# Performance work log

Hardware: AMD Instinct MI355X
Metric: run time of the kernel (lower is better)

Reference implementation:

```python
import jax, jax.numpy as jnp
import numpy as np

N_NODES = 50000
N_EDGES = 1600000
IN_FEATS = 32
HIDDEN = 64
OUT_FEAT = 64


def setup_inputs() -> dict:
    key = jax.random.key(0)
    ks = jax.random.split(key, 8)
    inputs = jax.random.normal(ks[0], (N_NODES, IN_FEATS), dtype=jnp.float32)
    edge_weights = jax.random.uniform(ks[1], (N_EDGES, 1), dtype=jnp.float32)
    src = jax.random.randint(ks[2], (N_EDGES,), 0, N_NODES, dtype=jnp.int32)
    dst = jax.random.randint(ks[3], (N_EDGES,), 0, N_NODES, dtype=jnp.int32)
    W1 = jax.random.normal(ks[4], (IN_FEATS, HIDDEN), dtype=jnp.float32) / np.sqrt(IN_FEATS)
    b1 = jnp.zeros((HIDDEN,), dtype=jnp.float32)
    W2 = jax.random.normal(ks[5], (HIDDEN + IN_FEATS, OUT_FEAT), dtype=jnp.float32) / np.sqrt(HIDDEN + IN_FEATS)
    b2 = jnp.zeros((OUT_FEAT,), dtype=jnp.float32)
    return {"inputs": inputs, "edge_weights": edge_weights, "src": src, "dst": dst,
            "W1": W1, "b1": b1, "W2": W2, "b2": b2}


def _weighted_graph_conv(x, W, b, src, dst, ew, src_norm, dst_norm, n_nodes):
    # x: [N, Din] -> [N, Dout]
    x = x @ W                               # dense projection
    x = x * src_norm                        # D_out^{-1/2} scaling at source
    m = x[src] * ew                         # [E, Dout] gather * edge weight
    h = jax.ops.segment_sum(m, dst, num_segments=n_nodes)  # scatter-sum at dest
    return h * dst_norm + b                 # D_in^{-1/2} scaling + bias


def reference(inputs, edge_weights, src, dst, W1, b1, W2, b2):
    n = inputs.shape[0]
    ones = jnp.ones((src.shape[0],), dtype=jnp.float32)
    out_deg = jax.ops.segment_sum(ones, src, num_segments=n)
    in_deg = jax.ops.segment_sum(ones, dst, num_segments=n)
    src_norm = jnp.clip(out_deg, 1.0, None)[:, None] ** -0.5  # [N,1]
    dst_norm = jnp.clip(in_deg, 1.0, None)[:, None] ** -0.5   # [N,1]

    h = _weighted_graph_conv(inputs, W1, b1, src, dst, edge_weights, src_norm, dst_norm, n)
    h = jax.nn.relu(h)
    reminder = jnp.concatenate([h, inputs], axis=-1)  # re-inject input features
    h = _weighted_graph_conv(reminder, W2, b2, src, dst, edge_weights, src_norm, dst_norm, n)
    h = jax.nn.relu(h)
    # torch F.normalize(p=2, dim=-1, eps=1e-12)
    norm = jnp.linalg.norm(h, axis=-1, keepdims=True)
    return h / jnp.maximum(norm, 1e-12)
```

## Files before the change

### kernel.cpp

```cpp
#include <hip/hip_runtime.h>
#include <math.h>


#define BUK 128
#define BUK_SHIFT 7
#define FSH 256
#define SS 128
#define HIST_BS 512
#define NBUK_MAX 512
#define MAX_LDS_BYTES 131072
#define PNB 16

#define SCAN_BS 256
#define SCAN_ITEMS 4
#define SCAN_CHUNK (SCAN_BS * SCAN_ITEMS)

__device__ __forceinline__ unsigned short f2bf(float f) {
    unsigned u = __float_as_uint(f);
    return (unsigned short)((u + 0x7fffu + ((u >> 16) & 1u)) >> 16);
}
__device__ __forceinline__ float bf2f(unsigned short h) {
    return __uint_as_float((unsigned)h << 16);
}

__device__ __forceinline__ float edge_gather(const int* __restrict__ offsets,
                                             const unsigned* __restrict__ edata,
                                             const unsigned short* __restrict__ xp,
                                             int n, int lane) {
    int beg = offsets[n];
    int end = offsets[n + 1];
    float a0 = 0.f, a1 = 0.f, a2 = 0.f, a3 = 0.f;
    for (int p = beg; p < end; p += 64) {
        int cnt = min(64, end - p);
        unsigned eb = (p + lane < end) ? edata[p + lane] : 0u;
        int k = 0;
        for (; k + 7 < cnt; k += 8) {
            unsigned e0 = __builtin_amdgcn_readlane(eb, k);
            unsigned e1 = __builtin_amdgcn_readlane(eb, k + 1);
            unsigned e2 = __builtin_amdgcn_readlane(eb, k + 2);
            unsigned e3 = __builtin_amdgcn_readlane(eb, k + 3);
            unsigned e4 = __builtin_amdgcn_readlane(eb, k + 4);
            unsigned e5 = __builtin_amdgcn_readlane(eb, k + 5);
            unsigned e6 = __builtin_amdgcn_readlane(eb, k + 6);
            unsigned e7 = __builtin_amdgcn_readlane(eb, k + 7);
            float v0 = bf2f(xp[(size_t)(e0 & 0xffffu) * 64 + lane]);
            float v1 = bf2f(xp[(size_t)(e1 & 0xffffu) * 64 + lane]);
            float v2 = bf2f(xp[(size_t)(e2 & 0xffffu) * 64 + lane]);
            float v3 = bf2f(xp[(size_t)(e3 & 0xffffu) * 64 + lane]);
            float v4 = bf2f(xp[(size_t)(e4 & 0xffffu) * 64 + lane]);
            float v5 = bf2f(xp[(size_t)(e5 & 0xffffu) * 64 + lane]);
            float v6 = bf2f(xp[(size_t)(e6 & 0xffffu) * 64 + lane]);
            float v7 = bf2f(xp[(size_t)(e7 & 0xffffu) * 64 + lane]);
            a0 = fmaf(v0, bf2f((unsigned short)(e0 >> 16)), a0);
            a1 = fmaf(v1, bf2f((unsigned short)(e1 >> 16)), a1);
            a2 = fmaf(v2, bf2f((unsigned short)(e2 >> 16)), a2);
            a3 = fmaf(v3, bf2f((unsigned short)(e3 >> 16)), a3);
            a0 = fmaf(v4, bf2f((unsigned short)(e4 >> 16)), a0);
            a1 = fmaf(v5, bf2f((unsigned short)(e5 >> 16)), a1);
            a2 = fmaf(v6, bf2f((unsigned short)(e6 >> 16)), a2);
            a3 = fmaf(v7, bf2f((unsigned short)(e7 >> 16)), a3);
        }
        for (; k < cnt; ++k) {
            unsigned e0 = __builtin_amdgcn_readlane(eb, k);
            a0 = fmaf(bf2f(xp[(size_t)(e0 & 0xffffu) * 64 + lane]),
                      bf2f((unsigned short)(e0 >> 16)), a0);
        }
    }
    return (a0 + a1) + (a2 + a3);
}

__global__ void hist_src_kernel(const int* __restrict__ src, unsigned* __restrict__ partial_s,
                                int E, int NW4, int sliceS) {
    extern __shared__ unsigned h[];
    for (int i = threadIdx.x; i < NW4; i += blockDim.x) h[i] = 0u;
    __syncthreads();
    int s = blockIdx.x;
    int beg = s * sliceS, end = min(beg + sliceS, E);
    for (int e = beg + (int)threadIdx.x; e < end; e += blockDim.x) {
        int v = src[e];
        atomicAdd(&h[v >> 2], 1u << (8 * (v & 3)));
    }
    __syncthreads();
    unsigned* o = partial_s + (size_t)s * NW4;
    for (int i = threadIdx.x; i < NW4; i += blockDim.x) o[i] = h[i];
}

__global__ void reduce_src_kernel(const unsigned* __restrict__ partial_s,
                                  float* __restrict__ srcn, int N, int NW4) {
    int w = blockIdx.x * blockDim.x + threadIdx.x;
    if (w >= NW4) return;
    unsigned run = 0;
#pragma unroll 4
    for (int s = 0; s < SS; ++s) run += partial_s[(size_t)s * NW4 + w];
    int n0 = 4 * w;
#pragma unroll
    for (int k = 0; k < 4; ++k) {
        int n = n0 + k;
        if (n < N) srcn[n] = rsqrtf(fmaxf((float)((run >> (8 * k)) & 0xffu), 1.0f));
    }
}

__global__ void count_kernel(const int* __restrict__ dst, int* __restrict__ cntmat,
                             int E, int L, int NBUK) {
    __shared__ int c[NBUK_MAX];
    for (int i = threadIdx.x; i < NBUK; i += blockDim.x) c[i] = 0;
    __syncthreads();
    int s = blockIdx.x;
    int beg = s * L, end = min(beg + L, E);
    for (int e = beg + (int)threadIdx.x; e < end; e += blockDim.x)
        atomicAdd(&c[dst[e] >> BUK_SHIFT], 1);
    __syncthreads();
    for (int b = threadIdx.x; b < NBUK; b += blockDim.x)
        cntmat[(size_t)b * FSH + s] = c[b];
}

__global__ void scan_partial(const int* __restrict__ deg, int* __restrict__ bsum, int N) {
    __shared__ int sdata[SCAN_BS];
    int t = threadIdx.x;
    int base = blockIdx.x * SCAN_CHUNK + t * SCAN_ITEMS;
    int s = 0;
#pragma unroll
    for (int k = 0; k < SCAN_ITEMS; ++k) {
        int idx = base + k;
        s += (idx < N) ? deg[idx] : 0;
    }
    sdata[t] = s;
    __syncthreads();
    for (int off = SCAN_BS / 2; off > 0; off >>= 1) {
        if (t < off) sdata[t] += sdata[t + off];
        __syncthreads();
    }
    if (t == 0) bsum[blockIdx.x] = sdata[0];
}

__global__ void scan_bsums(int* __restrict__ bsum, int NB) {
    int carry = 0;
    for (int base = 0; base < NB; base += 64) {
        int l = base + (int)threadIdx.x;
        int v = (l < NB) ? bsum[l] : 0;
        int inc = v;
#pragma unroll
        for (int off = 1; off < 64; off <<= 1) {
            int tv = __shfl_up(inc, off, 64);
            if ((int)threadIdx.x >= off) inc += tv;
        }
        if (l < NB) bsum[l] = carry + inc - v;
        carry += __shfl(inc, 63, 64);
    }
}

__global__ void scan_final(const int* __restrict__ deg, const int* __restrict__ bsum,
                           int* __restrict__ offsets, int N) {
    __shared__ int sdata[SCAN_BS];
    int t = threadIdx.x;
    int base = blockIdx.x * SCAN_CHUNK + t * SCAN_ITEMS;
    int loc[SCAN_ITEMS];
    int s = 0;
#pragma unroll
    for (int k = 0; k < SCAN_ITEMS; ++k) {
        int idx = base + k;
        loc[k] = (idx < N) ? deg[idx] : 0;
        s += loc[k];
    }
    sdata[t] = s;
    __syncthreads();
    for (int off = 1; off < SCAN_BS; off <<= 1) {
        int v = (t >= off) ? sdata[t - off] : 0;
        __syncthreads();
        sdata[t] += v;
        __syncthreads();
    }
    int excl = sdata[t] - s + bsum[blockIdx.x];
#pragma unroll
    for (int k = 0; k < SCAN_ITEMS; ++k) {
        int idx = base + k;
        if (idx < N) {
            offsets[idx] = excl;
            if (idx == N - 1) offsets[N] = excl + loc[k];
        }
        excl += loc[k];
    }
}

__global__ void place_seg_kernel(const int* __restrict__ src, const int* __restrict__ dst,
                                 const float* __restrict__ ew, const int* __restrict__ cscan,
                                 uint2* __restrict__ inter, int E, int L, int NBUK) {
    __shared__ int cur[NBUK_MAX];
    int s = blockIdx.x;
    for (int b = threadIdx.x; b < NBUK; b += blockDim.x)
        cur[b] = cscan[(size_t)b * FSH + s];
    __syncthreads();
    int beg = s * L, end = min(beg + L, E);
    for (int e = beg + (int)threadIdx.x; e < end; e += blockDim.x) {
        int d = dst[e];
        int b = d >> BUK_SHIFT;
        int pos = atomicAdd(&cur[b], 1);
        inter[pos] = make_uint2((unsigned)src[e] | ((unsigned)f2bf(ew[e]) << 16),
                                (unsigned)(d & (BUK - 1)));
    }
}

__global__ void fill_final_kernel(const uint2* __restrict__ inter,
                                  const int* __restrict__ cscan,
                                  unsigned* __restrict__ edata, int* __restrict__ offsets,
                                  float* __restrict__ dstn, int N, int NBUK) {
    __shared__ int cnt[BUK];
    __shared__ int loff[BUK];
    int b = blockIdx.x;
    int t = threadIdx.x;
    int beg = cscan[(size_t)b * FSH];
    int end = cscan[(size_t)(b + 1) * FSH];
    if (t < BUK) cnt[t] = 0;
    __syncthreads();
    for (int p = beg + t; p < end; p += blockDim.x)
        atomicAdd(&cnt[inter[p].y], 1);
    __syncthreads();
    if (t < 64) {
        int carry = 0;
#pragma unroll
        for (int base = 0; base < BUK; base += 64) {
            int v = cnt[base + t];
            int inc = v;
#pragma unroll
            for (int off = 1; off < 64; off <<= 1) {
                int tv = __shfl_up(inc, off, 64);
                if (t >= off) inc += tv;
            }
            loff[base + t] = carry + inc - v;
            carry += __shfl(inc, 63, 64);
        }
    }
    __syncthreads();
    int node0 = b << BUK_SHIFT;
    if (t < BUK) {
        int n = node0 + t;
        if (n < N) {
            offsets[n] = beg + loff[t];
            dstn[n] = rsqrtf(fmaxf((float)cnt[t], 1.0f));
        }
    }
    if (b == NBUK - 1 && t == 0) offsets[N] = end;
    __syncthreads();
    if (t < BUK) cnt[t] = 0;
    __syncthreads();
    for (int p = beg + t; p < end; p += blockDim.x) {
        uint2 r = inter[p];
        int dl = (int)r.y;
        int rk = atomicAdd(&cnt[dl], 1);
        edata[beg + loff[dl] + rk] = r.x;
    }
}

__global__ void proj1_kernel(const float* __restrict__ X, const float* __restrict__ W1,
                             const float* __restrict__ srcn,
                             unsigned short* __restrict__ xp, int N) {
    __shared__ float w[32 * 64];
    __shared__ float xs[PNB][32];
    int tid = threadIdx.x;
    {
        const float4* Wv = (const float4*)W1;
        float4* wv = (float4*)w;
        for (int i = tid; i < 32 * 64 / 4; i += 256) wv[i] = Wv[i];
    }
    int nodeBase = blockIdx.x * PNB;
    int nrows = min(PNB, N - nodeBase);
    {
        const float4* Xv = (const float4*)(X + (size_t)nodeBase * 32);
        float4* xv = (float4*)&xs[0][0];
        for (int i = tid; i < nrows * 8; i += 256) xv[i] = Xv[i];
    }
    __syncthreads();
    int lane = tid & 63;
    int wid = tid >> 6;
    int m0 = wid * 4;
    float acc[4] = {0.f, 0.f, 0.f, 0.f};
#pragma unroll
    for (int kk = 0; kk < 32; kk += 4) {
        float w0 = w[(kk + 0) * 64 + lane], w1 = w[(kk + 1) * 64 + lane];
        float w2 = w[(kk + 2) * 64 + lane], w3 = w[(kk + 3) * 64 + lane];
#pragma unroll
        for (int m = 0; m < 4; ++m) {
            float4 x = *(const float4*)&xs[m0 + m][kk];
            acc[m] = fmaf(x.x, w0, fmaf(x.y, w1, fmaf(x.z, w2, fmaf(x.w, w3, acc[m]))));
        }
    }
#pragma unroll
    for (int m = 0; m < 4; ++m) {
        int n = nodeBase + m0 + m;
        if (n < N) xp[(size_t)n * 64 + lane] = f2bf(acc[m] * srcn[n]);
    }
}

__global__ void __launch_bounds__(256, 8)
gp2_kernel(const int* __restrict__ offsets, const unsigned* __restrict__ edata,
           const unsigned short* __restrict__ xp, const float* __restrict__ dstn,
           const float* __restrict__ srcn, const float* __restrict__ b1,
           const float* __restrict__ X, const float* __restrict__ W2,
           unsigned short* __restrict__ xp2, int N) {
    __shared__ unsigned short w2[96 * 64];
    __shared__ float hrow[4][64];
    __shared__ float xrow[4][32];
    int tid = threadIdx.x;
    for (int i = tid; i < 96 * 64; i += 256) w2[i] = f2bf(W2[i]);
    __syncthreads();
    int lane = tid & 63;
    int wid = tid >> 6;
    for (int j = 0; j < 4; ++j) {
        int n = blockIdx.x * 16 + wid * 4 + j;
        if (n >= N) return;
        float acc = edge_gather(offsets, edata, xp, n, lane);
        float h = fmaxf(acc * dstn[n] + b1[lane], 0.0f);
        hrow[wid][lane] = h;
        if (lane < 32) xrow[wid][lane] = X[(size_t)n * 32 + lane];
        float p2 = 0.f;
#pragma unroll 8
        for (int k = 0; k < 64; ++k)
            p2 = fmaf(hrow[wid][k], bf2f(w2[k * 64 + lane]), p2);
#pragma unroll 8
        for (int k = 0; k < 32; ++k)
            p2 = fmaf(xrow[wid][k], bf2f(w2[(64 + k) * 64 + lane]), p2);
        xp2[(size_t)n * 64 + lane] = f2bf(p2 * srcn[n]);
    }
}

__global__ void __launch_bounds__(256, 8)
gather_final_kernel(const int* __restrict__ offsets, const unsigned* __restrict__ edata,
                    const unsigned short* __restrict__ xp2, const float* __restrict__ dstn,
                    const float* __restrict__ b2, float* __restrict__ out, int N) {
    int lane = threadIdx.x & 63;
    int n = blockIdx.x * 4 + (threadIdx.x >> 6);
    if (n >= N) return;
    float acc = edge_gather(offsets, edata, xp2, n, lane);
    float v = fmaxf(acc * dstn[n] + b2[lane], 0.0f);
    float s = v * v;
#pragma unroll
    for (int off = 32; off >= 1; off >>= 1) s += __shfl_xor(s, off, 64);
    v = v / fmaxf(sqrtf(s), 1e-12f);
    out[(size_t)n * 64 + lane] = v;
}

__global__ void deg_kernel_i(const int* __restrict__ src, const int* __restrict__ dst,
                             int* __restrict__ degs, int* __restrict__ degd, int E) {
    int i = blockIdx.x * blockDim.x + threadIdx.x;
    if (i < E) {
        atomicAdd(&degs[src[i]], 1);
        atomicAdd(&degd[dst[i]], 1);
    }
}

__global__ void norm_kernel_i(const int* __restrict__ degs, const int* __restrict__ degd,
                              float* __restrict__ srcn, float* __restrict__ dstn, int N) {
    int i = blockIdx.x * blockDim.x + threadIdx.x;
    if (i < N) {
        srcn[i] = rsqrtf(fmaxf((float)degs[i], 1.0f));
        dstn[i] = rsqrtf(fmaxf((float)degd[i], 1.0f));
    }
}

__global__ void proj2_kernel(const float* __restrict__ h, const float* __restrict__ X,
                             const float* __restrict__ W2, const float* __restrict__ srcn,
                             unsigned short* __restrict__ xp, int N) {
    __shared__ float w[96 * 64];
    __shared__ float xs[PNB][96];
    int tid = threadIdx.x;
    {
        const float4* Wv = (const float4*)W2;
        float4* wv = (float4*)w;
        for (int i = tid; i < 96 * 64 / 4; i += 256) wv[i] = Wv[i];
    }
    int nodeBase = blockIdx.x * PNB;
    int nrows = min(PNB, N - nodeBase);
    for (int i = tid; i < nrows * 16; i += 256) {
        int r = i >> 4, c = i & 15;
        *(float4*)&xs[r][c * 4] = *(const float4*)(h + (size_t)(nodeBase + r) * 64 + c * 4);
    }
    for (int i = tid; i < nrows * 8; i += 256) {
        int r = i >> 3, c = i & 7;
        *(float4*)&xs[r][64 + c * 4] = *(const float4*)(X + (size_t)(nodeBase + r) * 32 + c * 4);
    }
    __syncthreads();
    int lane = tid & 63;
    int wid = tid >> 6;
    int m0 = wid * 4;
    float acc[4] = {0.f, 0.f, 0.f, 0.f};
#pragma unroll 6
    for (int kk = 0; kk < 96; kk += 4) {
        float w0 = w[(kk + 0) * 64 + lane], w1 = w[(kk + 1) * 64 + lane];
        float w2 = w[(kk + 2) * 64 + lane], w3 = w[(kk + 3) * 64 + lane];
#pragma unroll
        for (int m = 0; m < 4; ++m) {
            float4 x = *(const float4*)&xs[m0 + m][kk];
            acc[m] = fmaf(x.x, w0, fmaf(x.y, w1, fmaf(x.z, w2, fmaf(x.w, w3, acc[m]))));
        }
    }
#pragma unroll
    for (int m = 0; m < 4; ++m) {
        int n = nodeBase + m0 + m;
        if (n < N) xp[(size_t)n * 64 + lane] = f2bf(acc[m] * srcn[n]);
    }
}

__global__ void scatter_kernel(const int* __restrict__ src, const int* __restrict__ dst,
                               const float* __restrict__ ew,
                               const unsigned short* __restrict__ xp,
                               float* __restrict__ acc, int E) {
    int total = E * 64;
    int stride = gridDim.x * blockDim.x;
    for (int i = blockIdx.x * blockDim.x + threadIdx.x; i < total; i += stride) {
        int e = i >> 6;
        int f = i & 63;
        int s = src[e];
        int d = dst[e];
        float v = bf2f(xp[(size_t)s * 64 + f]) * ew[e];
        atomicAdd(&acc[(size_t)d * 64 + f], v);
    }
}

__global__ void relu_bias_kernel(float* __restrict__ h, const float* __restrict__ dstn,
                                 const float* __restrict__ b, int N) {
    int i = blockIdx.x * blockDim.x + threadIdx.x;
    if (i < N * 64) {
        int n = i >> 6;
        int j = i & 63;
        h[i] = fmaxf(h[i] * dstn[n] + b[j], 0.0f);
    }
}

__global__ void finalize_kernel(float* __restrict__ out, const float* __restrict__ dstn,
                                const float* __restrict__ b, int N) {
    int i = blockIdx.x * blockDim.x + threadIdx.x;
    int n = i >> 6;
    int f = i & 63;
    if (n >= N) return;
    float v = fmaxf(out[(size_t)n * 64 + f] * dstn[n] + b[f], 0.0f);
    float s = v * v;
#pragma unroll
    for (int off = 32; off >= 1; off >>= 1) s += __shfl_xor(s, off, 64);
    out[(size_t)n * 64 + f] = v / fmaxf(sqrtf(s), 1e-12f);
}


extern "C" void kernel_launch(void* const* d_in, const int* in_sizes, int n_in,
                              void* d_out, int out_size, void* d_ws, size_t ws_size,
                              hipStream_t stream) {
    const float* X   = (const float*)d_in[0];
    const float* ew  = (const float*)d_in[1];
    const int*   src = (const int*)d_in[2];
    const int*   dst = (const int*)d_in[3];
    const float* W1  = (const float*)d_in[4];
    const float* b1  = (const float*)d_in[5];
    const float* W2  = (const float*)d_in[6];
    const float* b2  = (const float*)d_in[7];

    const int N = in_sizes[0] / 32;
    const int E = in_sizes[2];
    const int NW4 = (N + 3) / 4;
    const int NBUK = (N + BUK - 1) / BUK;
    const int M = NBUK * FSH;
    const int L = (E + FSH - 1) / FSH;
    const int sliceS = (E + SS - 1) / SS;
    const int NBscan = (M + SCAN_CHUNK - 1) / SCAN_CHUNK;
    const int projGrid = (N + PNB - 1) / PNB;

    float* out = (float*)d_out;
    char* wsb = (char*)d_ws;

    size_t o = 0;
    auto alloc = [&](size_t bytes) { size_t p = o; o += (bytes + 255) & ~(size_t)255; return p; };
    size_t szPS = (size_t)SS * NW4 * 4;
    size_t szIN = (size_t)E * 8;
    size_t szXP = (size_t)N * 64 * 2;
    size_t szI = szPS > szIN ? szPS : szIN; if (szXP > szI) szI = szXP;
    size_t offI    = alloc(szI);
    size_t offEd   = alloc((size_t)E * 4);
    size_t offXP2  = alloc((size_t)N * 64 * 2);
    size_t offCS   = alloc(((size_t)M + 1) * 4);
    size_t offSrcn = alloc((size_t)N * 4);
    size_t offDstn = alloc((size_t)N * 4);
    size_t offOff  = alloc(((size_t)N + 1) * 4);
    size_t offBsum = alloc((size_t)NBscan * 4);
    size_t need = o;

    bool ok = (ws_size >= need) && (N <= 65536) && (NBUK <= NBUK_MAX) &&
              ((size_t)NW4 * 4 <= MAX_LDS_BYTES);

    if (ok) {
        unsigned*       partial_s = (unsigned*)(wsb + offI);
        uint2*          inter     = (uint2*)(wsb + offI);
        unsigned short* xp        = (unsigned short*)(wsb + offI);
        unsigned*       edata     = (unsigned*)(wsb + offEd);
        unsigned short* xp2       = (unsigned short*)(wsb + offXP2);
        int*            cscan     = (int*)(wsb + offCS);
        float*          srcn      = (float*)(wsb + offSrcn);
        float*          dstn      = (float*)(wsb + offDstn);
        int*            offsets   = (int*)(wsb + offOff);
        int*            bsum      = (int*)(wsb + offBsum);

        hist_src_kernel<<<SS, HIST_BS, (size_t)NW4 * 4, stream>>>(src, partial_s, E, NW4, sliceS);
        reduce_src_kernel<<<(NW4 + 255) / 256, 256, 0, stream>>>(partial_s, srcn, N, NW4);

        count_kernel<<<FSH, HIST_BS, 0, stream>>>(dst, cscan, E, L, NBUK);
        scan_partial<<<NBscan, SCAN_BS, 0, stream>>>(cscan, bsum, M);
        scan_bsums<<<1, 64, 0, stream>>>(bsum, NBscan);
        scan_final<<<NBscan, SCAN_BS, 0, stream>>>(cscan, bsum, cscan, M);
        place_seg_kernel<<<FSH, HIST_BS, 0, stream>>>(src, dst, ew, cscan, inter, E, L, NBUK);
        fill_final_kernel<<<NBUK, 256, 0, stream>>>(inter, cscan, edata, offsets, dstn, N, NBUK);

        proj1_kernel<<<projGrid, 256, 0, stream>>>(X, W1, srcn, xp, N);
        gp2_kernel<<<(N + 15) / 16, 256, 0, stream>>>(offsets, edata, xp, dstn, srcn, b1,
                                                      X, W2, xp2, N);
        gather_final_kernel<<<(N + 3) / 4, 256, 0, stream>>>(offsets, edata, xp2, dstn,
                                                             b2, out, N);
    } else {
        float* ws   = (float*)d_ws;
        int*   degs = (int*)ws;
        int*   degd = (int*)(ws + N);
        float* srcn = ws + 2 * (size_t)N;
        float* dstn = ws + 3 * (size_t)N;
        unsigned short* xp = (unsigned short*)(ws + 4 * (size_t)N);

        hipMemsetAsync(degs, 0, 2 * (size_t)N * sizeof(float), stream);
        hipMemsetAsync(out, 0, (size_t)N * 64 * sizeof(float), stream);

        deg_kernel_i<<<(E + 255) / 256, 256, 0, stream>>>(src, dst, degs, degd, E);
        norm_kernel_i<<<(N + 255) / 256, 256, 0, stream>>>(degs, degd, srcn, dstn, N);

        proj1_kernel<<<projGrid, 256, 0, stream>>>(X, W1, srcn, xp, N);
        scatter_kernel<<<2048, 256, 0, stream>>>(src, dst, ew, xp, out, E);
        relu_bias_kernel<<<(N * 64 + 255) / 256, 256, 0, stream>>>(out, dstn, b1, N);

        proj2_kernel<<<projGrid, 256, 0, stream>>>(out, X, W2, srcn, xp, N);
        hipMemsetAsync(out, 0, (size_t)N * 64 * sizeof(float), stream);
        scatter_kernel<<<2048, 256, 0, stream>>>(src, dst, ew, xp, out, E);
        finalize_kernel<<<(N * 64 + 255) / 256, 256, 0, stream>>>(out, dstn, b2, N);
    }
}
```

Measured before the change: 197.4 us.

## Split fused layer-1 gather and layer-2 projection into separate kernels

Replaces the fused gp2 kernel, which gathered each node's neighbours and then ran a per-node 96x64 matvec from LDS, with two kernels. The first only gathers and stores the ReLU hidden state as bf16. The second is a tiled projection that stages fp32 W2 and 16 rows of [h, X] in LDS and computes 4 rows per wave. The aim is to avoid the serial per-node matvec inside the latency-bound gather and to raise occupancy of the gather kernel, at the cost of an extra bf16 hidden buffer round-trip through memory and one more launch. The hidden state is now rounded to bf16 before projection.

```diff
diff --git a/kernel.cpp b/kernel.cpp
--- a/kernel.cpp
+++ b/kernel.cpp
@@ -292,34 +292,62 @@
 }
 
 __global__ void __launch_bounds__(256, 8)
-gp2_kernel(const int* __restrict__ offsets, const unsigned* __restrict__ edata,
-           const unsigned short* __restrict__ xp, const float* __restrict__ dstn,
-           const float* __restrict__ srcn, const float* __restrict__ b1,
-           const float* __restrict__ X, const float* __restrict__ W2,
-           unsigned short* __restrict__ xp2, int N) {
-    __shared__ unsigned short w2[96 * 64];
-    __shared__ float hrow[4][64];
-    __shared__ float xrow[4][32];
+gather_h_kernel(const int* __restrict__ offsets, const unsigned* __restrict__ edata,
+                const unsigned short* __restrict__ xp, const float* __restrict__ dstn,
+                const float* __restrict__ b1, unsigned short* __restrict__ hout, int N) {
+    int lane = threadIdx.x & 63;
+    int n = blockIdx.x * 4 + (threadIdx.x >> 6);
+    if (n >= N) return;
+    float acc = edge_gather(offsets, edata, xp, n, lane);
+    float v = fmaxf(acc * dstn[n] + b1[lane], 0.0f);
+    hout[(size_t)n * 64 + lane] = f2bf(v);
+}
+
+__global__ void proj2b_kernel(const unsigned short* __restrict__ h,
+                              const float* __restrict__ X,
+                              const float* __restrict__ W2, const float* __restrict__ srcn,
+                              unsigned short* __restrict__ xp2, int N) {
+    __shared__ float w[96 * 64];
+    __shared__ float xs[PNB][96];
     int tid = threadIdx.x;
-    for (int i = tid; i < 96 * 64; i += 256) w2[i] = f2bf(W2[i]);
+    {
+        const float4* Wv = (const float4*)W2;
+        float4* wv = (float4*)w;
+        for (int i = tid; i < 96 * 64 / 4; i += 256) wv[i] = Wv[i];
+    }
+    int nodeBase = blockIdx.x * PNB;
+    int nrows = min(PNB, N - nodeBase);
+    for (int i = tid; i < nrows * 16; i += 256) {
+        int r = i >> 4, c = i & 15;
+        ushort4 v = *(const ushort4*)(h + (size_t)(nodeBase + r) * 64 + c * 4);
+        xs[r][c * 4 + 0] = bf2f(v.x);
+        xs[r][c * 4 + 1] = bf2f(v.y);
+        xs[r][c * 4 + 2] = bf2f(v.z);
+        xs[r][c * 4 + 3] = bf2f(v.w);
+    }
+    for (int i = tid; i < nrows * 8; i += 256) {
+        int r = i >> 3, c = i & 7;
+        *(float4*)&xs[r][64 + c * 4] = *(const float4*)(X + (size_t)(nodeBase + r) * 32 + c * 4);
+    }
     __syncthreads();
     int lane = tid & 63;
     int wid = tid >> 6;
-    for (int j = 0; j < 4; ++j) {
-        int n = blockIdx.x * 16 + wid * 4 + j;
-        if (n >= N) return;
-        float acc = edge_gather(offsets, edata, xp, n, lane);
-        float h = fmaxf(acc * dstn[n] + b1[lane], 0.0f);
-        hrow[wid][lane] = h;
-        if (lane < 32) xrow[wid][lane] = X[(size_t)n * 32 + lane];
-        float p2 = 0.f;
-#pragma unroll 8
-        for (int k = 0; k < 64; ++k)
-            p2 = fmaf(hrow[wid][k], bf2f(w2[k * 64 + lane]), p2);
-#pragma unroll 8
-        for (int k = 0; k < 32; ++k)
-            p2 = fmaf(xrow[wid][k], bf2f(w2[(64 + k) * 64 + lane]), p2);
-        xp2[(size_t)n * 64 + lane] = f2bf(p2 * srcn[n]);
+    int m0 = wid * 4;
+    float acc[4] = {0.f, 0.f, 0.f, 0.f};
+#pragma unroll 6
+    for (int kk = 0; kk < 96; kk += 4) {
+        float w0 = w[(kk + 0) * 64 + lane], w1 = w[(kk + 1) * 64 + lane];
+        float w2 = w[(kk + 2) * 64 + lane], w3 = w[(kk + 3) * 64 + lane];
+#pragma unroll
+        for (int m = 0; m < 4; ++m) {
+            float4 x = *(const float4*)&xs[m0 + m][kk];
+            acc[m] = fmaf(x.x, w0, fmaf(x.y, w1, fmaf(x.z, w2, fmaf(x.w, w3, acc[m]))));
+        }
+    }
+#pragma unroll
+    for (int m = 0; m < 4; ++m) {
+        int n = nodeBase + m0 + m;
+        if (n < N) xp2[(size_t)n * 64 + lane] = f2bf(acc[m] * srcn[n]);
     }
 }
 
@@ -469,8 +497,10 @@
     auto alloc = [&](size_t bytes) { size_t p = o; o += (bytes + 255) & ~(size_t)255; return p; };
     size_t szPS = (size_t)SS * NW4 * 4;
     size_t szIN = (size_t)E * 8;
-    size_t szXP = (size_t)N * 64 * 2;
-    size_t szI = szPS > szIN ? szPS : szIN; if (szXP > szI) szI = szXP;
+    size_t szXP = ((size_t)N * 64 * 2 + 255) & ~(size_t)255;
+    size_t szH  = (size_t)N * 64 * 2;
+    size_t szI = szPS > szIN ? szPS : szIN;
+    if (szXP + szH > szI) szI = szXP + szH;
     size_t offI    = alloc(szI);
     size_t offEd   = alloc((size_t)E * 4);
     size_t offXP2  = alloc((size_t)N * 64 * 2);
@@ -488,6 +518,7 @@
         unsigned*       partial_s = (unsigned*)(wsb + offI);
         uint2*          inter     = (uint2*)(wsb + offI);
         unsigned short* xp        = (unsigned short*)(wsb + offI);
+        unsigned short* hbuf      = (unsigned short*)(wsb + offI + szXP);
         unsigned*       edata     = (unsigned*)(wsb + offEd);
         unsigned short* xp2       = (unsigned short*)(wsb + offXP2);
         int*            cscan     = (int*)(wsb + offCS);
@@ -507,8 +538,8 @@
         fill_final_kernel<<<NBUK, 256, 0, stream>>>(inter, cscan, edata, offsets, dstn, N, NBUK);
 
         proj1_kernel<<<projGrid, 256, 0, stream>>>(X, W1, srcn, xp, N);
-        gp2_kernel<<<(N + 15) / 16, 256, 0, stream>>>(offsets, edata, xp, dstn, srcn, b1,
-                                                      X, W2, xp2, N);
+        gather_h_kernel<<<(N + 3) / 4, 256, 0, stream>>>(offsets, edata, xp, dstn, b1, hbuf, N);
+        proj2b_kernel<<<projGrid, 256, 0, stream>>>(hbuf, X, W2, srcn, xp2, N);
         gather_final_kernel<<<(N + 3) / 4, 256, 0, stream>>>(offsets, edata, xp2, dstn,
                                                              b2, out, N);
     } else {
```

Result: no change. 197.4 us (-0.0%).
